# Performance work log

Measured on AMD Instinct MI355X. Metric: run time of the kernel, lower is better.

## Reference

```python
import jax, jax.numpy as jnp
import numpy as np

B = 4096      # batch of edges
D = 512       # high-dim feature size
E_DIM = 2     # visualization embedding dim
G = 1024      # number of unique edge_from rows (groups)
BIG = 1e9     # padding value pushed to end of sorts
LAMBD = 1.0
EPS = 1e-12


def setup_inputs() -> dict:
    key = jax.random.key(0)
    ks = jax.random.split(key, 7)
    pool = jax.random.normal(ks[0], (G, D), jnp.float32)
    gid = jax.random.randint(ks[1], (B,), 0, G)
    edge_from = pool[gid]  # duplicated rows -> groups, as the module expects
    edge_to = jax.random.normal(ks[2], (B, D), jnp.float32)
    embedding_to = jax.random.normal(ks[3], (B, E_DIM), jnp.float32)
    embedding_from = jax.random.normal(ks[4], (B, E_DIM), jnp.float32)
    recon_to = jax.random.normal(ks[5], (B, D), jnp.float32)
    recon_from = jax.random.normal(ks[6], (B, D), jnp.float32)
    return {
        "edge_to": edge_to, "edge_from": edge_from,
        "embedding_to": embedding_to, "embedding_from": embedding_from,
        "recon_to": recon_to, "recon_from": recon_from,
    }


def _pairwise_dist(x):
    # Euclidean pairwise distances via Gram matrix; safe sqrt (clip handles
    # rounding-negative values and the exact-zero diagonal).
    n = jnp.sum(x * x, axis=-1)
    d2 = n[:, None] + n[None, :] - 2.0 * (x @ x.T)
    return jnp.sqrt(jnp.clip(d2, EPS, None))


def batch_ranking_loss(edge_from, edge_to, embedding_from, embedding_to):
    b = edge_from.shape[0]
    # Group membership: rows of edge_from that are identical (squared distance 0).
    ef = jax.lax.stop_gradient(edge_from)
    n = jnp.sum(ef * ef, axis=-1)
    d2f = n[:, None] + n[None, :] - 2.0 * (ef @ ef.T)
    same = d2f < 1e-3                       # [B, B] bool, includes diagonal
    k = jnp.sum(same, axis=-1)              # group size per anchor row
    rep = jnp.argmax(same, axis=-1)         # first member index = group id

    d_high = jnp.where(same, _pairwise_dist(edge_to), BIG)
    d_low = jnp.where(same, _pairwise_dist(embedding_to), BIG)

    order = jnp.argsort(d_high, axis=-1)                      # rank by high-dim dist
    gathered = jnp.take_along_axis(d_low, order, axis=-1)     # low-dim dists in high order
    s = jnp.sort(gathered, axis=-1)                           # ascending; BIG pads at end
    diffs = jax.nn.relu(s[:, 1:] - s[:, :-1])                 # [B, B-1]
    pos = jnp.arange(b - 1)
    valid = pos[None, :] < (k[:, None] - 1)                   # only real-member diffs
    row = jnp.sum(jnp.where(valid, diffs, 0.0), axis=-1) / jnp.maximum(k - 1, 1)

    # Average rows within each group, then average over groups with >= 2 members.
    sum_r = jax.ops.segment_sum(row, rep, num_segments=b)
    cnt = jax.ops.segment_sum(jnp.ones((b,), row.dtype), rep, num_segments=b)
    is_group = cnt >= 2.0
    group_loss = jnp.where(is_group, sum_r / jnp.maximum(cnt, 1.0), 0.0)
    n_valid = jnp.sum(is_group.astype(row.dtype))
    return jnp.sum(group_loss) / jnp.maximum(n_valid, 1.0)


def _umap_loss(embedding_to, embedding_from):
    # Stand-in attraction term: mean log(1 + ||e_to - e_from||^2).
    d2 = jnp.sum((embedding_to - embedding_from) ** 2, axis=-1)
    return jnp.mean(jnp.log1p(d2))


def _recon_loss(edge_to, edge_from, recon_to, recon_from):
    return jnp.mean((recon_to - edge_to) ** 2) + jnp.mean((recon_from - edge_from) ** 2)


def reference(edge_to, edge_from, embedding_to, embedding_from, recon_to, recon_from):
    umap_l = _umap_loss(embedding_to, embedding_from)
    recon_l = _recon_loss(edge_to, edge_from, recon_to, recon_from)
    rank_l = batch_ranking_loss(edge_from, edge_to, embedding_from, embedding_to)
    total = umap_l + LAMBD * recon_l + rank_l
    return (umap_l, recon_l, rank_l, total)
```

## Files before the change

### kernel.cpp

```cpp
#include <hip/hip_runtime.h>
#include <stdint.h>

#define NB 4096
#define ND 512
#define K1_GRID 1024
#define RPB 4
#define K2_GRID (NB / RPB)
#define BLK 256

static_assert(K1_GRID * 4 == NB, "one edge_from row per wave");
static_assert(K2_GRID * RPB == NB, "rank rows cover batch");

static constexpr float kEps = 1e-12f;

__device__ inline uint64_t splitmix64(uint64_t x) {
    x += 0x9E3779B97F4A7C15ULL;
    x = (x ^ (x >> 30)) * 0xBF58476D1CE4E5B9ULL;
    x = (x ^ (x >> 27)) * 0x94D049BB133111EBULL;
    return x ^ (x >> 31);
}

__global__ __launch_bounds__(BLK) void k_pre(
        const float4* __restrict__ edge_to4,
        const float*  __restrict__ edge_from,
        const float2* __restrict__ emb_to,
        const float2* __restrict__ emb_from,
        const float4* __restrict__ recon_to4,
        const float*  __restrict__ recon_from,
        uint64_t* __restrict__ hash,
        float* __restrict__ recon_part,
        float* __restrict__ umap_part,
        unsigned int* __restrict__ counter)
{
    const int tid  = threadIdx.x;
    const int b    = blockIdx.x;
    const int wave = tid >> 6, lane = tid & 63;

    if (b == 0 && tid == 0) atomicExch(counter, 0u);

    const int row = b * 4 + wave;
    const uint4*  ef4 = reinterpret_cast<const uint4*>(edge_from  + (size_t)row * ND);
    const float4* rf4 = reinterpret_cast<const float4*>(recon_from + (size_t)row * ND);
    uint4  ua = ef4[lane * 2], ub = ef4[lane * 2 + 1];
    float4 ra = rf4[lane * 2], rb = rf4[lane * 2 + 1];
    uint32_t wbits[8] = {ua.x, ua.y, ua.z, ua.w, ub.x, ub.y, ub.z, ub.w};
    float    rvals[8] = {ra.x, ra.y, ra.z, ra.w, rb.x, rb.y, rb.z, rb.w};
    uint64_t h = 0;
    float    s = 0.f;
    const int base = lane * 8;
    #pragma unroll
    for (int t = 0; t < 8; ++t) {
        h += splitmix64((uint64_t)wbits[t] ^ ((uint64_t)(base + t) * 0xA24BAED4963EE407ULL));
        float d = rvals[t] - __uint_as_float(wbits[t]);
        s = fmaf(d, d, s);
    }
    {
        const int i0 = b * 512 + tid;
        #pragma unroll
        for (int q = 0; q < 2; ++q) {
            const int i = i0 + q * 256;
            float4 a = edge_to4[i], c = recon_to4[i];
            float t1;
            t1 = c.x - a.x; s = fmaf(t1, t1, s);
            t1 = c.y - a.y; s = fmaf(t1, t1, s);
            t1 = c.z - a.z; s = fmaf(t1, t1, s);
            t1 = c.w - a.w; s = fmaf(t1, t1, s);
        }
    }
    float uml = 0.f;
    if (tid < 4) {
        const int i = b * 4 + tid;
        float2 a = emb_to[i], c = emb_from[i];
        float dx = a.x - c.x, dy = a.y - c.y;
        uml = log1pf(fmaf(dx, dx, dy * dy));
    }
    #pragma unroll
    for (int off = 32; off; off >>= 1) h += __shfl_down(h, off, 64);
    if (lane == 0) hash[row] = h;
    #pragma unroll
    for (int off = 32; off; off >>= 1) s += __shfl_down(s, off, 64);
    if (wave == 0) {
        uml += __shfl_down(uml, 2, 64);
        uml += __shfl_down(uml, 1, 64);
    }
    __shared__ float sws[4];
    if (lane == 0) sws[wave] = s;
    __syncthreads();
    if (tid == 0) {
        recon_part[b] = sws[0] + sws[1] + sws[2] + sws[3];
        umap_part[b]  = uml;
    }
}

__global__ __launch_bounds__(BLK) void k_rank_fin(
        const uint64_t* __restrict__ hash,
        const float2* __restrict__ emb,
        const float* __restrict__ recon_part,
        const float* __restrict__ umap_part,
        float* __restrict__ vpart,
        float* __restrict__ npart,
        unsigned int* __restrict__ counter,
        float* __restrict__ out)
{
    __shared__ uint64_t sh[NB];
    const int tid = threadIdx.x;
    for (int j = tid; j < NB; j += BLK) sh[j] = hash[j];
    __syncthreads();

    const int wave = tid >> 6, lane = tid & 63;
    const int row  = blockIdx.x * RPB + wave;
    const uint64_t hrow = sh[row];
    const float2 ei = emb[row];

    int   cnt = 0, minj = NB;
    float d2max = -1.0f, d2min = 1e30f;
    #pragma unroll 4
    for (int j = lane; j < NB; j += 64) {
        const bool m = (sh[j] == hrow);
        const float2 ej = emb[j];
        const float dx = ei.x - ej.x, dy = ei.y - ej.y;
        const float d2 = fmaf(dx, dx, dy * dy);
        cnt  += m ? 1 : 0;
        minj  = (m && j < minj) ? j : minj;
        d2max = (m && d2 > d2max) ? d2 : d2max;
        d2min = (m && d2 < d2min) ? d2 : d2min;
    }
    #pragma unroll
    for (int off = 32; off; off >>= 1) {
        cnt  += __shfl_down(cnt, off, 64);
        minj  = min(minj, __shfl_down(minj, off, 64));
        d2max = fmaxf(d2max, __shfl_down(d2max, off, 64));
        d2min = fminf(d2min, __shfl_down(d2min, off, 64));
    }
    __shared__ float svw[4], snw[4];
    if (lane == 0) {
        if (cnt >= 2) {
            const float dmax = sqrtf(fmaxf(d2max, kEps));
            const float dmin = sqrtf(fmaxf(d2min, kEps));
            svw[wave] = ((dmax - dmin) / (float)(cnt - 1)) / (float)cnt;
            snw[wave] = (minj == row) ? 1.0f : 0.0f;
        } else { svw[wave] = 0.f; snw[wave] = 0.f; }
    }
    __syncthreads();
    __shared__ bool is_last;
    if (tid == 0) {
        vpart[blockIdx.x] = svw[0] + svw[1] + svw[2] + svw[3];
        npart[blockIdx.x] = snw[0] + snw[1] + snw[2] + snw[3];
        __threadfence();
        unsigned int t = atomicAdd(counter, 1u);
        is_last = (t == K2_GRID - 1);
    }
    __syncthreads();
    if (!is_last) return;
    __threadfence();

    double r = 0.0, u = 0.0, v = 0.0, nv = 0.0;
    for (int i = tid; i < K1_GRID; i += BLK) { r += (double)recon_part[i];
                                               u += (double)umap_part[i]; }
    for (int i = tid; i < K2_GRID; i += BLK) { v += (double)vpart[i];
                                               nv += (double)npart[i]; }
    #pragma unroll
    for (int off = 32; off; off >>= 1) {
        r += __shfl_down(r, off, 64);  u  += __shfl_down(u, off, 64);
        v += __shfl_down(v, off, 64);  nv += __shfl_down(nv, off, 64);
    }
    __shared__ double sr[4], su[4], sv[4], sn[4];
    const int lane2 = tid & 63, wid = tid >> 6;
    if (lane2 == 0) { sr[wid] = r; su[wid] = u; sv[wid] = v; sn[wid] = nv; }
    __syncthreads();
    if (tid == 0) {
        double R = sr[0] + sr[1] + sr[2] + sr[3];
        double U = su[0] + su[1] + su[2] + su[3];
        double V = sv[0] + sv[1] + sv[2] + sv[3];
        double N = sn[0] + sn[1] + sn[2] + sn[3];
        double umap  = U / (double)NB;
        double recon = R / ((double)NB * (double)ND);
        double rank  = V / (N > 1.0 ? N : 1.0);
        out[0] = (float)umap;
        out[1] = (float)recon;
        out[2] = (float)rank;
        out[3] = (float)(umap + recon + rank);
    }
}

extern "C" void kernel_launch(void* const* d_in, const int* in_sizes, int n_in,
                              void* d_out, int out_size, void* d_ws, size_t ws_size,
                              hipStream_t stream) {
    const float4* edge_to4   = (const float4*)d_in[0];
    const float*  edge_from  = (const float*)d_in[1];
    const float2* emb_to     = (const float2*)d_in[2];
    const float2* emb_from   = (const float2*)d_in[3];
    const float4* recon_to4  = (const float4*)d_in[4];
    const float*  recon_from = (const float*)d_in[5];

    char* ws = (char*)d_ws;
    uint64_t* hash       = (uint64_t*)ws;  ws += (size_t)NB * 8;
    float*    recon_part = (float*)ws;     ws += (size_t)K1_GRID * 4;
    float*    umap_part  = (float*)ws;     ws += (size_t)K1_GRID * 4;
    float*    vpart      = (float*)ws;     ws += (size_t)K2_GRID * 4;
    float*    npart      = (float*)ws;     ws += (size_t)K2_GRID * 4;
    unsigned int* counter = (unsigned int*)ws;

    k_pre<<<K1_GRID, BLK, 0, stream>>>(
        edge_to4, edge_from, emb_to, emb_from, recon_to4, recon_from,
        hash, recon_part, umap_part, counter);
    k_rank_fin<<<K2_GRID, BLK, 0, stream>>>(
        hash, emb_to, recon_part, umap_part, vpart, npart, counter, (float*)d_out);
}
```

Before: 46.37 us.

## Group rows with an atomic hash table instead of all-pairs hash comparison

Rows of edge_from are now inserted into a global open-addressing hash table during the preprocessing kernel, recording up to 32 member row indices per group. The rank kernel then processes one group per wave, working only over its members via shuffles. This replaces the previous design, where each of 1024 blocks loaded all 4096 hashes into LDS and scanned them. The cost is an extra memset, global atomics in the first kernel, and a hard cap of 32 members per group, which would silently truncate larger groups.

```diff
diff --git a/kernel.cpp b/kernel.cpp
--- a/kernel.cpp
+++ b/kernel.cpp
@@ -4,12 +4,12 @@
 #define NB 4096
 #define ND 512
 #define K1_GRID 1024
-#define RPB 4
-#define K2_GRID (NB / RPB)
+#define TBL 4096
+#define MAXK 32
+#define K2_GRID (TBL / 4)
 #define BLK 256
 
 static_assert(K1_GRID * 4 == NB, "one edge_from row per wave");
-static_assert(K2_GRID * RPB == NB, "rank rows cover batch");
 
 static constexpr float kEps = 1e-12f;
 
@@ -27,7 +27,9 @@
         const float2* __restrict__ emb_from,
         const float4* __restrict__ recon_to4,
         const float*  __restrict__ recon_from,
-        uint64_t* __restrict__ hash,
+        unsigned long long* __restrict__ tableH,
+        unsigned int* __restrict__ gcount,
+        int* __restrict__ gmember,
         float* __restrict__ recon_part,
         float* __restrict__ umap_part,
         unsigned int* __restrict__ counter)
@@ -76,7 +78,17 @@
     }
     #pragma unroll
     for (int off = 32; off; off >>= 1) h += __shfl_down(h, off, 64);
-    if (lane == 0) hash[row] = h;
+    if (lane == 0) {
+        unsigned long long hh = (unsigned long long)h;
+        unsigned slot = (unsigned)hh & (TBL - 1);
+        while (true) {
+            unsigned long long prev = atomicCAS(&tableH[slot], 0ULL, hh);
+            if (prev == 0ULL || prev == hh) break;
+            slot = (slot + 1) & (TBL - 1);
+        }
+        unsigned pos = atomicAdd(&gcount[slot], 1u);
+        if (pos < MAXK) gmember[slot * MAXK + pos] = row;
+    }
     #pragma unroll
     for (int off = 32; off; off >>= 1) s += __shfl_down(s, off, 64);
     if (wave == 0) {
@@ -93,7 +105,8 @@
 }
 
 __global__ __launch_bounds__(BLK) void k_rank_fin(
-        const uint64_t* __restrict__ hash,
+        const unsigned int* __restrict__ gcount,
+        const int* __restrict__ gmember,
         const float2* __restrict__ emb,
         const float* __restrict__ recon_part,
         const float* __restrict__ umap_part,
@@ -102,45 +115,49 @@
         unsigned int* __restrict__ counter,
         float* __restrict__ out)
 {
-    __shared__ uint64_t sh[NB];
     const int tid = threadIdx.x;
-    for (int j = tid; j < NB; j += BLK) sh[j] = hash[j];
-    __syncthreads();
-
     const int wave = tid >> 6, lane = tid & 63;
-    const int row  = blockIdx.x * RPB + wave;
-    const uint64_t hrow = sh[row];
-    const float2 ei = emb[row];
-
-    int   cnt = 0, minj = NB;
-    float d2max = -1.0f, d2min = 1e30f;
-    #pragma unroll 4
-    for (int j = lane; j < NB; j += 64) {
-        const bool m = (sh[j] == hrow);
-        const float2 ej = emb[j];
-        const float dx = ei.x - ej.x, dy = ei.y - ej.y;
-        const float d2 = fmaf(dx, dx, dy * dy);
-        cnt  += m ? 1 : 0;
-        minj  = (m && j < minj) ? j : minj;
-        d2max = (m && d2 > d2max) ? d2 : d2max;
-        d2min = (m && d2 < d2min) ? d2 : d2min;
-    }
-    #pragma unroll
-    for (int off = 32; off; off >>= 1) {
-        cnt  += __shfl_down(cnt, off, 64);
-        minj  = min(minj, __shfl_down(minj, off, 64));
-        d2max = fmaxf(d2max, __shfl_down(d2max, off, 64));
-        d2min = fminf(d2min, __shfl_down(d2min, off, 64));
-    }
-    __shared__ float svw[4], snw[4];
-    if (lane == 0) {
-        if (cnt >= 2) {
+    const int slot = blockIdx.x * 4 + wave;
+
+    const unsigned k = gcount[slot];
+    float v = 0.f, nvf = 0.f;
+    if (k >= 2u) {
+        const int kk = (int)min(k, (unsigned)MAXK);
+        const bool act = lane < kk;
+        int myrow = act ? gmember[slot * MAXK + lane] : 0x7FFFFFFF;
+        int rnk = 0;
+        for (int j = 0; j < kk; ++j) {
+            int rj = __shfl(myrow, j, 64);
+            if (act && rj < myrow) ++rnk;
+        }
+        int srow = 0x7FFFFFFF;
+        for (int j = 0; j < kk; ++j) {
+            int rj = __shfl(myrow, j, 64);
+            int pj = __shfl(rnk, j, 64);
+            if (pj == lane) srow = rj;
+        }
+        float ex = 0.f, ey = 0.f;
+        if (act) { float2 e = emb[srow]; ex = e.x; ey = e.y; }
+        float d2max = -1.f, d2min = 1e30f;
+        for (int j = 0; j < kk; ++j) {
+            float xj = __shfl(ex, j, 64), yj = __shfl(ey, j, 64);
+            float dx = ex - xj, dy = ey - yj;
+            float d2 = fmaf(dx, dx, dy * dy);
+            d2max = fmaxf(d2max, d2);
+            d2min = fminf(d2min, d2);
+        }
+        float row_i = 0.f;
+        if (act) {
             const float dmax = sqrtf(fmaxf(d2max, kEps));
             const float dmin = sqrtf(fmaxf(d2min, kEps));
-            svw[wave] = ((dmax - dmin) / (float)(cnt - 1)) / (float)cnt;
-            snw[wave] = (minj == row) ? 1.0f : 0.0f;
-        } else { svw[wave] = 0.f; snw[wave] = 0.f; }
-    }
+            row_i = (dmax - dmin) / (float)(k - 1u);
+        }
+        #pragma unroll
+        for (int off = 32; off; off >>= 1) row_i += __shfl_down(row_i, off, 64);
+        if (lane == 0) { v = row_i / (float)k; nvf = 1.f; }
+    }
+    __shared__ float svw[4], snw[4];
+    if (lane == 0) { svw[wave] = v; snw[wave] = nvf; }
     __syncthreads();
     __shared__ bool is_last;
     if (tid == 0) {
@@ -154,19 +171,19 @@
     if (!is_last) return;
     __threadfence();
 
-    double r = 0.0, u = 0.0, v = 0.0, nv = 0.0;
+    double r = 0.0, u = 0.0, vv = 0.0, nv = 0.0;
     for (int i = tid; i < K1_GRID; i += BLK) { r += (double)recon_part[i];
                                                u += (double)umap_part[i]; }
-    for (int i = tid; i < K2_GRID; i += BLK) { v += (double)vpart[i];
+    for (int i = tid; i < K2_GRID; i += BLK) { vv += (double)vpart[i];
                                                nv += (double)npart[i]; }
     #pragma unroll
     for (int off = 32; off; off >>= 1) {
-        r += __shfl_down(r, off, 64);  u  += __shfl_down(u, off, 64);
-        v += __shfl_down(v, off, 64);  nv += __shfl_down(nv, off, 64);
+        r  += __shfl_down(r, off, 64);  u  += __shfl_down(u, off, 64);
+        vv += __shfl_down(vv, off, 64); nv += __shfl_down(nv, off, 64);
     }
     __shared__ double sr[4], su[4], sv[4], sn[4];
     const int lane2 = tid & 63, wid = tid >> 6;
-    if (lane2 == 0) { sr[wid] = r; su[wid] = u; sv[wid] = v; sn[wid] = nv; }
+    if (lane2 == 0) { sr[wid] = r; su[wid] = u; sv[wid] = vv; sn[wid] = nv; }
     __syncthreads();
     if (tid == 0) {
         double R = sr[0] + sr[1] + sr[2] + sr[3];
@@ -194,16 +211,21 @@
     const float*  recon_from = (const float*)d_in[5];
 
     char* ws = (char*)d_ws;
-    uint64_t* hash       = (uint64_t*)ws;  ws += (size_t)NB * 8;
-    float*    recon_part = (float*)ws;     ws += (size_t)K1_GRID * 4;
-    float*    umap_part  = (float*)ws;     ws += (size_t)K1_GRID * 4;
-    float*    vpart      = (float*)ws;     ws += (size_t)K2_GRID * 4;
-    float*    npart      = (float*)ws;     ws += (size_t)K2_GRID * 4;
-    unsigned int* counter = (unsigned int*)ws;
+    unsigned long long* tableH = (unsigned long long*)ws;  ws += (size_t)TBL * 8;
+    unsigned int* gcount       = (unsigned int*)ws;        ws += (size_t)TBL * 4;
+    int*          gmember      = (int*)ws;                 ws += (size_t)TBL * MAXK * 4;
+    float*        recon_part   = (float*)ws;               ws += (size_t)K1_GRID * 4;
+    float*        umap_part    = (float*)ws;               ws += (size_t)K1_GRID * 4;
+    float*        vpart        = (float*)ws;               ws += (size_t)K2_GRID * 4;
+    float*        npart        = (float*)ws;               ws += (size_t)K2_GRID * 4;
+    unsigned int* counter      = (unsigned int*)ws;
+
+    hipMemsetAsync(tableH, 0, (size_t)TBL * 8 + (size_t)TBL * 4, stream);
 
     k_pre<<<K1_GRID, BLK, 0, stream>>>(
         edge_to4, edge_from, emb_to, emb_from, recon_to4, recon_from,
-        hash, recon_part, umap_part, counter);
+        tableH, gcount, gmember, recon_part, umap_part, counter);
     k_rank_fin<<<K2_GRID, BLK, 0, stream>>>(
-        hash, emb_to, recon_part, umap_part, vpart, npart, counter, (float*)d_out);
-}
+        gcount, gmember, emb_to, recon_part, umap_part,
+        vpart, npart, counter, (float*)d_out);
+}
```

Measured after the change: 40.41 us. 12.8% less time.
